# Kernel tuning notes

Hardware: AMD Instinct MI355X
Metric: run time of the kernel (lower is better)

## Reference

```python
import jax, jax.numpy as jnp
import numpy as np

# Static problem constants (see shape_source)
T_, H_, W_ = 8, 37, 37          # frames, feature-map height/width (518/14)
NH, MP = 8, 8                   # num_heads, max_points


def _point_mask_np():
    # n_points(t, r) = max(1, int(MP * (1 - |t-r|/(T-1)))) as in the TxT loop.
    d = np.abs(np.arange(T_)[:, None] - np.arange(T_)[None, :])
    n_p = np.maximum(1, (MP * (1.0 - d / (T_ - 1))).astype(np.int64))
    return np.arange(MP)[None, None, :] < n_p[:, :, None]   # [T, T, P] bool


def setup_inputs() -> dict:
    key = jax.random.key(0)
    ks = jax.random.split(key, 4)
    B, T, N, C = 2, T_, H_ * W_, 384
    f_bt = jax.random.normal(ks[0], (B, T, N, C), jnp.float32)
    Wq = 0.05 * jax.random.normal(ks[1], (C, C), jnp.float32)
    Woff = 0.1 * jax.random.normal(ks[2], (C, NH * MP * 2), jnp.float32)  # offsets span a few pixels
    Wout = 0.05 * jax.random.normal(ks[3], (C, C), jnp.float32)
    return {
        'f_bt': f_bt,
        'Wq': Wq, 'bq': jnp.zeros((C,), jnp.float32),
        'Woff': Woff, 'boff': jnp.zeros((NH * MP * 2,), jnp.float32),
        'Wout': Wout, 'bout': jnp.zeros((C,), jnp.float32),
    }


def _forward(f_bt, Wq, bq, Woff, boff, Wout, bout):
    B, T, N, C = f_bt.shape
    h, P = NH, MP
    hd = C // h
    scale = hd ** -0.5
    H, W = H_, W_

    # Per-frame projections (query and offsets depend only on t, computed once).
    q = (f_bt @ Wq + bq).reshape(B, T, N, h, hd)                 # [B,T,N,h,hd]
    off = (f_bt @ Woff + boff).reshape(B, T, N, h, P, 2)         # [B,T,N,h,P,2]

    ys, xs = jnp.meshgrid(jnp.arange(H), jnp.arange(W), indexing='ij')
    coords = jnp.stack([ys, xs], -1).reshape(N, 2).astype(f_bt.dtype)
    # Sampling locations in pixel space (align_corners=True normalize+denormalize is identity).
    loc = coords[None, None, :, None, None, :] + off             # [B,T,N,h,P,2]

    # Reference frames as per-head channel images, flattened spatially.
    ref = f_bt.transpose(0, 1, 3, 2).reshape(B, T, h, hd, N)     # [B,T,h,hd,H*W]
    mask = jnp.asarray(_point_mask_np())                         # [T,T,P]

    def attend(q_t, loc_t, mask_t):
        # q_t: [B,N,h,hd], loc_t: [B,N,h,P,2], mask_t: [T,P]
        y = loc_t[..., 0]
        x = loc_t[..., 1]
        y0f = jnp.floor(y)
        x0f = jnp.floor(x)
        wy = y - y0f
        wx = x - x0f

        def gather(yf, xf, w):
            yi = yf.astype(jnp.int32)
            xi = xf.astype(jnp.int32)
            valid = ((yi >= 0) & (yi < H) & (xi >= 0) & (xi < W)).astype(q_t.dtype)
            idx = jnp.clip(yi, 0, H - 1) * W + jnp.clip(xi, 0, W - 1)     # [B,N,h,P]
            idx = idx.transpose(0, 2, 1, 3).reshape(B, 1, h, 1, N * P)
            idx = jnp.broadcast_to(idx, (B, T, h, 1, N * P))
            vals = jnp.take_along_axis(ref, idx, axis=4)                   # [B,T,h,hd,N*P]
            vals = vals.reshape(B, T, h, hd, N, P)
            wv = (w * valid).transpose(0, 2, 1, 3)[:, None, :, None, :, :]  # [B,1,h,1,N,P]
            return vals * wv

        # Bilinear sample (zeros padding) of every reference frame at the
        # offset-predicted points of frame t.
        s = (gather(y0f, x0f, (1 - wy) * (1 - wx))
             + gather(y0f, x0f + 1, (1 - wy) * wx)
             + gather(y0f + 1, x0f, wy * (1 - wx))
             + gather(y0f + 1, x0f + 1, wy * wx))                # [B,T,h,hd,N,P]

        logits = jnp.einsum('bnhd,brhdnp->brnhp', q_t, s) * scale
        logits = logits + jnp.where(mask_t[None, :, None, None, :], 0.0, -1e30)
        attn = jax.nn.softmax(logits, axis=-1)
        out = jnp.einsum('brnhp,brhdnp->brnhd', attn, s).mean(axis=1)  # avg over T refs
        return out.reshape(B, N, C) @ Wout + bout

    body = jax.checkpoint(attend)

    def step(carry, xs):
        q_t, loc_t, mask_t = xs
        return carry, body(q_t, loc_t, mask_t)

    _, fused = jax.lax.scan(
        step, None,
        (q.transpose(1, 0, 2, 3, 4), loc.transpose(1, 0, 2, 3, 4, 5), mask))
    return fused.transpose(1, 0, 2, 3)   # [B,T,N,C]


def reference(f_bt, Wq, bq, Woff, boff, Wout, bout):
    return _forward(f_bt, Wq, bq, Woff, boff, Wout, bout)
```

## Files before the change

### kernel.cpp

```cpp
#include <hip/hip_runtime.h>
#include <hip/hip_bf16.h>
#include <hip/hip_fp16.h>
#include <cstddef>

constexpr int B_  = 2;
constexpr int T_  = 8;
constexpr int HW_ = 37;
constexpr int N_  = HW_ * HW_;
constexpr int C_  = 384;
constexpr int NH_ = 8;
constexpr int MP_ = 8;
constexpr int HD_ = C_ / NH_;
constexpr int M_  = B_ * T_ * N_;

typedef short bf16x8 __attribute__((ext_vector_type(8)));
typedef float f32x4 __attribute__((ext_vector_type(4)));
typedef float f32x2 __attribute__((ext_vector_type(2)));
typedef _Float16 h16x2 __attribute__((ext_vector_type(2)));
typedef unsigned u32x3 __attribute__((ext_vector_type(3)));
typedef u32x3 uau32x3 __attribute__((aligned(4)));

static __device__ __forceinline__ unsigned short bf16_bits(float v) {
  __hip_bfloat16 b = __float2bfloat16(v);
  return *reinterpret_cast<unsigned short*>(&b);
}

static __device__ __forceinline__ h16x2 bch2(unsigned u) {
  return __builtin_bit_cast(h16x2, u);
}

__global__ __launch_bounds__(256)
void cast_transpose_kernel(const float* __restrict__ f,
                           __hip_bfloat16* __restrict__ A16,
                           _Float16* __restrict__ ft) {
  const int bn = blockIdx.x;
  const int n = bn % N_;
  const int b = bn / N_;
  const size_t dst_base = (size_t)bn * (T_ * C_);
#pragma unroll
  for (int i = 0; i < 12; ++i) {
    int idx = i * 256 + threadIdx.x;
    int t = idx / C_;
    int c = idx - t * C_;
    size_t src = ((size_t)(b * T_ + t) * N_ + n) * C_ + c;
    float v = f[src];
    ft[dst_base + idx] = (_Float16)v;
    A16[src] = __float2bfloat16(v);
  }
}

__global__ __launch_bounds__(256)
void prep_w_kernel(const float* __restrict__ Wq, const float* __restrict__ Woff,
                   const float* __restrict__ Wout,
                   __hip_bfloat16* __restrict__ Wt, __hip_bfloat16* __restrict__ Wot) {
  int nrow = blockIdx.x;
  if (nrow < 512) {
    const float* src; int col, ld;
    if (nrow < 384) { src = Wq; col = nrow; ld = 384; }
    else            { src = Woff; col = nrow - 384; ld = 128; }
    for (int k = threadIdx.x; k < 384; k += 256)
      Wt[(size_t)nrow * 384 + k] = __float2bfloat16(src[(size_t)k * ld + col]);
  } else {
    int col = nrow - 512;
    for (int k = threadIdx.x; k < 384; k += 256)
      Wot[(size_t)col * 384 + k] = __float2bfloat16(Wout[(size_t)k * 384 + col]);
  }
}

__global__ __launch_bounds__(256)
void mfma_gemm_kernel(const __hip_bfloat16* __restrict__ A,
                      const __hip_bfloat16* __restrict__ Wt,
                      const float* __restrict__ b0, const float* __restrict__ b1,
                      float* __restrict__ out0, _Float16* __restrict__ out0h,
                      float* __restrict__ out1,
                      int split, float out0_scale) {
  __shared__ __hip_bfloat16 As[128][40];
  __shared__ __hip_bfloat16 Bs[128][40];
  const int m0 = blockIdx.x * 128;
  const int n0 = blockIdx.y * 128;
  const int tid = threadIdx.x;
  const int wv = tid >> 6, lane = tid & 63;
  const int wr = wv >> 1, wc = wv & 1;
  const int lr = lane & 15, kg = lane >> 4;

  f32x4 acc[4][4] = {};

  for (int k0 = 0; k0 < 384; k0 += 32) {
#pragma unroll
    for (int u = 0; u < 2; ++u) {
      int c = tid + u * 256;
      int row = c >> 2;
      int off = (c & 3) * 8;
      int gm = m0 + row;
      uint4 va = make_uint4(0u, 0u, 0u, 0u);
      if (gm < M_) va = *(const uint4*)(A + (size_t)gm * 384 + k0 + off);
      *(uint4*)&As[row][off] = va;
      uint4 vb = *(const uint4*)(Wt + (size_t)(n0 + row) * 384 + k0 + off);
      *(uint4*)&Bs[row][off] = vb;
    }
    __syncthreads();

    bf16x8 af[4], bfr[4];
#pragma unroll
    for (int i = 0; i < 4; ++i)
      af[i] = *(const bf16x8*)&As[wr * 64 + i * 16 + lr][kg * 8];
#pragma unroll
    for (int i = 0; i < 4; ++i)
      bfr[i] = *(const bf16x8*)&Bs[wc * 64 + i * 16 + lr][kg * 8];

#pragma unroll
    for (int mi = 0; mi < 4; ++mi)
#pragma unroll
      for (int ni = 0; ni < 4; ++ni)
        acc[mi][ni] = __builtin_amdgcn_mfma_f32_16x16x32_bf16(
            af[mi], bfr[ni], acc[mi][ni], 0, 0, 0);
    __syncthreads();
  }

  const int mrow = (lane >> 4) * 4;
#pragma unroll
  for (int mi = 0; mi < 4; ++mi) {
#pragma unroll
    for (int ni = 0; ni < 4; ++ni) {
#pragma unroll
      for (int j = 0; j < 4; ++j) {
        int gm = m0 + wr * 64 + mi * 16 + mrow + j;
        int gn = n0 + wc * 64 + ni * 16 + lr;
        if (gm >= M_) continue;
        float v = acc[mi][ni][j];
        if (!split) {
          out0[(size_t)gm * 384 + gn] = (v + b0[gn]) * out0_scale;
        } else {
          if (gn < 384) out0h[(size_t)gm * 384 + gn] =
              (_Float16)((v + b0[gn]) * out0_scale);
          else          out1[(size_t)gm * 128 + (gn - 384)] = v + b1[gn - 384];
        }
      }
    }
  }
}

__global__ __launch_bounds__(256)
void attend_kernel(const _Float16* __restrict__ ft,
                   const _Float16* __restrict__ Qh,
                   const float* __restrict__ OFF,
                   __hip_bfloat16* __restrict__ O1) {
  const int grid = B_ * N_ * 2;
  const int q8 = grid / 8, r8 = grid % 8;
  int c = blockIdx.x & 7, j = blockIdx.x >> 3;
  int id = (c < r8) ? c * (q8 + 1) + j : r8 * (q8 + 1) + (c - r8) * q8 + j;
  const int hq = id & 1;
  const int bn = id >> 1;

  const int n = bn % N_;
  const int b = bn / N_;
  const int w    = threadIdx.x >> 6;
  const int h    = hq * 4 + w;
  const int lane = threadIdx.x & 63;
  const int p = lane >> 3;
  const int k = lane & 7;
  const float cy = (float)(n / HW_);
  const float cx = (float)(n % HW_);
  const int bnb = b * N_;
  const int chb = h * HD_ + 6 * k;

  for (int t = 0; t < T_; ++t) {
    const size_t row = (size_t)(b * T_ + t) * N_ + n;

    uau32x3 qw = *(const uau32x3*)(Qh + row * C_ + h * HD_ + 6 * k);
    h16x2 q01 = bch2(qw.x), q23 = bch2(qw.y), q45 = bch2(qw.z);

    const float* op = OFF + row * (NH_ * MP_ * 2) + h * (MP_ * 2) + p * 2;
    float y = cy + op[0];
    float x = cx + op[1];
    float y0f = floorf(y), x0f = floorf(x);
    float wy = y - y0f, wx = x - x0f;
    int y0 = (int)y0f, x0 = (int)x0f;
    int y1 = y0 + 1, x1 = x0 + 1;
    float vy0 = (y0 >= 0 && y0 < HW_) ? 1.f : 0.f;
    float vy1 = (y1 >= 0 && y1 < HW_) ? 1.f : 0.f;
    float vx0 = (x0 >= 0 && x0 < HW_) ? 1.f : 0.f;
    float vx1 = (x1 >= 0 && x1 < HW_) ? 1.f : 0.f;
    int cy0 = min(max(y0, 0), HW_ - 1), cy1 = min(max(y1, 0), HW_ - 1);
    int cx0 = min(max(x0, 0), HW_ - 1), cx1 = min(max(x1, 0), HW_ - 1);
    float tw0 = (1.f - wy) * (1.f - wx) * vy0 * vx0;
    float tw1 = (1.f - wy) * wx * vy0 * vx1;
    float tw2 = wy * (1.f - wx) * vy1 * vx0;
    float tw3 = wy * wx * vy1 * vx1;
    _Float16 t0h = (_Float16)tw0, t1h = (_Float16)tw1;
    _Float16 t2h = (_Float16)tw2, t3h = (_Float16)tw3;
    h16x2 tw0h = {t0h, t0h}, tw1h = {t1h, t1h};
    h16x2 tw2h = {t2h, t2h}, tw3h = {t3h, t3h};

    const _Float16* tp0 = ft + ((bnb + cy0 * HW_ + cx0) * T_ + 3) * C_ + chb;
    const _Float16* tp1 = ft + ((bnb + cy0 * HW_ + cx1) * T_ + 3) * C_ + chb;
    const _Float16* tp2 = ft + ((bnb + cy1 * HW_ + cx0) * T_ + 3) * C_ + chb;
    const _Float16* tp3 = ft + ((bnb + cy1 * HW_ + cx1) * T_ + 3) * C_ + chb;

    float o0 = 0.f, o1 = 0.f, o2 = 0.f, o3 = 0.f, o4 = 0.f, o5 = 0.f;

#pragma unroll
    for (int r = 0; r < T_; ++r) {
      const int roff = (r - 3) * C_;
      uau32x3 ua = *(const uau32x3*)(tp0 + roff);
      uau32x3 ub = *(const uau32x3*)(tp1 + roff);
      uau32x3 uc = *(const uau32x3*)(tp2 + roff);
      uau32x3 ud = *(const uau32x3*)(tp3 + roff);

      h16x2 s01 = bch2(ua.x) * tw0h + bch2(ub.x) * tw1h + bch2(uc.x) * tw2h + bch2(ud.x) * tw3h;
      h16x2 s23 = bch2(ua.y) * tw0h + bch2(ub.y) * tw1h + bch2(uc.y) * tw2h + bch2(ud.y) * tw3h;
      h16x2 s45 = bch2(ua.z) * tw0h + bch2(ub.z) * tw1h + bch2(uc.z) * tw2h + bch2(ud.z) * tw3h;

      float lg = __builtin_amdgcn_fdot2(q01, s01,
                 __builtin_amdgcn_fdot2(q23, s23,
                 __builtin_amdgcn_fdot2(q45, s45, 0.f, false), false), false);
      lg += __shfl_xor(lg, 1);
      lg += __shfl_xor(lg, 2);
      lg += __shfl_xor(lg, 4);

      int dd = t - r; dd = dd < 0 ? -dd : dd;
      int npts = (56 - 8 * dd) / 7; npts = npts < 1 ? 1 : npts;

      float e = (p < npts) ? exp2f(lg) : 0.f;
      float ssum = e;
      ssum += __shfl_xor(ssum, 8);
      ssum += __shfl_xor(ssum, 16);
      ssum += __shfl_xor(ssum, 32);
      float attn = e * __builtin_amdgcn_rcpf(ssum);

      o0 = fmaf((float)s01.x, attn, o0);
      o1 = fmaf((float)s01.y, attn, o1);
      o2 = fmaf((float)s23.x, attn, o2);
      o3 = fmaf((float)s23.y, attn, o3);
      o4 = fmaf((float)s45.x, attn, o4);
      o5 = fmaf((float)s45.y, attn, o5);
    }

    o0 += __shfl_xor(o0, 8); o0 += __shfl_xor(o0, 16); o0 += __shfl_xor(o0, 32);
    o1 += __shfl_xor(o1, 8); o1 += __shfl_xor(o1, 16); o1 += __shfl_xor(o1, 32);
    o2 += __shfl_xor(o2, 8); o2 += __shfl_xor(o2, 16); o2 += __shfl_xor(o2, 32);
    o3 += __shfl_xor(o3, 8); o3 += __shfl_xor(o3, 16); o3 += __shfl_xor(o3, 32);
    o4 += __shfl_xor(o4, 8); o4 += __shfl_xor(o4, 16); o4 += __shfl_xor(o4, 32);
    o5 += __shfl_xor(o5, 8); o5 += __shfl_xor(o5, 16); o5 += __shfl_xor(o5, 32);

    if (p == 0) {
      __hip_bfloat16* outp = O1 + row * C_ + h * HD_ + 6 * k;
      unsigned* u = (unsigned*)outp;
      u[0] = (unsigned)bf16_bits(o0 * 0.125f) | ((unsigned)bf16_bits(o1 * 0.125f) << 16);
      u[1] = (unsigned)bf16_bits(o2 * 0.125f) | ((unsigned)bf16_bits(o3 * 0.125f) << 16);
      u[2] = (unsigned)bf16_bits(o4 * 0.125f) | ((unsigned)bf16_bits(o5 * 0.125f) << 16);
    }
  }
}

extern "C" void kernel_launch(void* const* d_in, const int* in_sizes, int n_in,
                              void* d_out, int out_size, void* d_ws, size_t ws_size,
                              hipStream_t stream) {
  const float* f    = (const float*)d_in[0];
  const float* Wq   = (const float*)d_in[1];
  const float* bq   = (const float*)d_in[2];
  const float* Woff = (const float*)d_in[3];
  const float* boff = (const float*)d_in[4];
  const float* Wout = (const float*)d_in[5];
  const float* bout = (const float*)d_in[6];
  float* outp = (float*)d_out;

  _Float16* Qh = (_Float16*)d_ws;
  float* OFFb = (float*)(Qh + (size_t)M_ * C_);
  _Float16* ft = (_Float16*)(OFFb + (size_t)M_ * 128);
  __hip_bfloat16* A16 = (__hip_bfloat16*)(ft + (size_t)B_ * N_ * T_ * C_);
  __hip_bfloat16* O1  = A16;
  __hip_bfloat16* Wt  = A16 + (size_t)M_ * C_;
  __hip_bfloat16* Wot = Wt + (size_t)512 * 384;

  dim3 blk(256);

  cast_transpose_kernel<<<dim3(B_ * N_), blk, 0, stream>>>(f, A16, ft);
  prep_w_kernel<<<dim3(896), blk, 0, stream>>>(Wq, Woff, Wout, Wt, Wot);

  mfma_gemm_kernel<<<dim3((M_ + 127) / 128, 4), blk, 0, stream>>>(
      A16, Wt, bq, boff, nullptr, Qh, OFFb, 1, 0.20822825268806912f);

  attend_kernel<<<dim3(B_ * N_ * 2), blk, 0, stream>>>(ft, Qh, OFFb, O1);

  mfma_gemm_kernel<<<dim3((M_ + 127) / 128, 3), blk, 0, stream>>>(
      O1, Wot, bout, nullptr, outp, nullptr, nullptr, 0, 1.0f);
}
```

Measured before the change: 323.0 us.

## Remap attend lanes to 4 channel groups x 8 points x 2 ref halves, accumulate in fp16

Reassigns each wavefront's lanes so that each lane covers 12 channels (4 lanes per head) and one of two reference-frame halves. The r loop drops from 8 to 4 iterations per lane, and the logit reduction needs fewer shuffles. The output accumulators become packed fp16 and are reduced with packed shuffles across points and ref halves, which halves the shuffle count. The cost is lower precision in the attention-weighted sum, since fp16 now accumulates across 64 terms, and more registers per lane for the wider loads.

```diff
diff --git a/kernel.cpp b/kernel.cpp
--- a/kernel.cpp
+++ b/kernel.cpp
@@ -27,6 +27,12 @@
 
 static __device__ __forceinline__ h16x2 bch2(unsigned u) {
   return __builtin_bit_cast(h16x2, u);
+}
+
+static __device__ __forceinline__ h16x2 pk_shfl_add(h16x2 v, int mask) {
+  unsigned u = __builtin_bit_cast(unsigned, v);
+  unsigned w = __shfl_xor(u, mask);
+  return v + __builtin_bit_cast(h16x2, w);
 }
 
 __global__ __launch_bounds__(256)
@@ -157,18 +163,22 @@
   const int w    = threadIdx.x >> 6;
   const int h    = hq * 4 + w;
   const int lane = threadIdx.x & 63;
-  const int p = lane >> 3;
-  const int k = lane & 7;
+  const int k4 = lane & 3;
+  const int p  = (lane >> 2) & 7;
+  const int rh = lane >> 5;
   const float cy = (float)(n / HW_);
   const float cx = (float)(n % HW_);
   const int bnb = b * N_;
-  const int chb = h * HD_ + 6 * k;
+  const int chb = h * HD_ + 12 * k4;
 
   for (int t = 0; t < T_; ++t) {
     const size_t row = (size_t)(b * T_ + t) * N_ + n;
 
-    uau32x3 qw = *(const uau32x3*)(Qh + row * C_ + h * HD_ + 6 * k);
-    h16x2 q01 = bch2(qw.x), q23 = bch2(qw.y), q45 = bch2(qw.z);
+    const _Float16* qp = Qh + row * C_ + chb;
+    uau32x3 qa = *(const uau32x3*)qp;
+    uau32x3 qb = *(const uau32x3*)(qp + 6);
+    h16x2 q0 = bch2(qa.x), q1 = bch2(qa.y), q2 = bch2(qa.z);
+    h16x2 q3 = bch2(qb.x), q4 = bch2(qb.y), q5 = bch2(qb.z);
 
     const float* op = OFF + row * (NH_ * MP_ * 2) + h * (MP_ * 2) + p * 2;
     float y = cy + op[0];
@@ -192,63 +202,79 @@
     h16x2 tw0h = {t0h, t0h}, tw1h = {t1h, t1h};
     h16x2 tw2h = {t2h, t2h}, tw3h = {t3h, t3h};
 
-    const _Float16* tp0 = ft + ((bnb + cy0 * HW_ + cx0) * T_ + 3) * C_ + chb;
-    const _Float16* tp1 = ft + ((bnb + cy0 * HW_ + cx1) * T_ + 3) * C_ + chb;
-    const _Float16* tp2 = ft + ((bnb + cy1 * HW_ + cx0) * T_ + 3) * C_ + chb;
-    const _Float16* tp3 = ft + ((bnb + cy1 * HW_ + cx1) * T_ + 3) * C_ + chb;
-
-    float o0 = 0.f, o1 = 0.f, o2 = 0.f, o3 = 0.f, o4 = 0.f, o5 = 0.f;
-
-#pragma unroll
-    for (int r = 0; r < T_; ++r) {
-      const int roff = (r - 3) * C_;
-      uau32x3 ua = *(const uau32x3*)(tp0 + roff);
-      uau32x3 ub = *(const uau32x3*)(tp1 + roff);
-      uau32x3 uc = *(const uau32x3*)(tp2 + roff);
-      uau32x3 ud = *(const uau32x3*)(tp3 + roff);
-
-      h16x2 s01 = bch2(ua.x) * tw0h + bch2(ub.x) * tw1h + bch2(uc.x) * tw2h + bch2(ud.x) * tw3h;
-      h16x2 s23 = bch2(ua.y) * tw0h + bch2(ub.y) * tw1h + bch2(uc.y) * tw2h + bch2(ud.y) * tw3h;
-      h16x2 s45 = bch2(ua.z) * tw0h + bch2(ub.z) * tw1h + bch2(uc.z) * tw2h + bch2(ud.z) * tw3h;
-
-      float lg = __builtin_amdgcn_fdot2(q01, s01,
-                 __builtin_amdgcn_fdot2(q23, s23,
-                 __builtin_amdgcn_fdot2(q45, s45, 0.f, false), false), false);
+    const _Float16* tp0 = ft + ((size_t)(bnb + cy0 * HW_ + cx0) * T_ + rh + 3) * C_ + chb;
+    const _Float16* tp1 = ft + ((size_t)(bnb + cy0 * HW_ + cx1) * T_ + rh + 3) * C_ + chb;
+    const _Float16* tp2 = ft + ((size_t)(bnb + cy1 * HW_ + cx0) * T_ + rh + 3) * C_ + chb;
+    const _Float16* tp3 = ft + ((size_t)(bnb + cy1 * HW_ + cx1) * T_ + rh + 3) * C_ + chb;
+
+    h16x2 o0 = {(_Float16)0.f, (_Float16)0.f}, o1 = o0, o2 = o0,
+          o3 = o0, o4 = o0, o5 = o0;
+
+#pragma unroll
+    for (int i = 0; i < 4; ++i) {
+      const int roff = (2 * i - 3) * C_;
+      uau32x3 a0 = *(const uau32x3*)(tp0 + roff);
+      uau32x3 a1 = *(const uau32x3*)(tp0 + roff + 6);
+      uau32x3 b0 = *(const uau32x3*)(tp1 + roff);
+      uau32x3 b1 = *(const uau32x3*)(tp1 + roff + 6);
+      uau32x3 c0 = *(const uau32x3*)(tp2 + roff);
+      uau32x3 c1 = *(const uau32x3*)(tp2 + roff + 6);
+      uau32x3 d0 = *(const uau32x3*)(tp3 + roff);
+      uau32x3 d1 = *(const uau32x3*)(tp3 + roff + 6);
+
+      h16x2 s0 = bch2(a0.x) * tw0h + bch2(b0.x) * tw1h + bch2(c0.x) * tw2h + bch2(d0.x) * tw3h;
+      h16x2 s1 = bch2(a0.y) * tw0h + bch2(b0.y) * tw1h + bch2(c0.y) * tw2h + bch2(d0.y) * tw3h;
+      h16x2 s2 = bch2(a0.z) * tw0h + bch2(b0.z) * tw1h + bch2(c0.z) * tw2h + bch2(d0.z) * tw3h;
+      h16x2 s3 = bch2(a1.x) * tw0h + bch2(b1.x) * tw1h + bch2(c1.x) * tw2h + bch2(d1.x) * tw3h;
+      h16x2 s4 = bch2(a1.y) * tw0h + bch2(b1.y) * tw1h + bch2(c1.y) * tw2h + bch2(d1.y) * tw3h;
+      h16x2 s5 = bch2(a1.z) * tw0h + bch2(b1.z) * tw1h + bch2(c1.z) * tw2h + bch2(d1.z) * tw3h;
+
+      float lg = __builtin_amdgcn_fdot2(q0, s0,
+                 __builtin_amdgcn_fdot2(q1, s1,
+                 __builtin_amdgcn_fdot2(q2, s2,
+                 __builtin_amdgcn_fdot2(q3, s3,
+                 __builtin_amdgcn_fdot2(q4, s4,
+                 __builtin_amdgcn_fdot2(q5, s5, 0.f, false),
+                 false), false), false), false), false);
+
       lg += __shfl_xor(lg, 1);
       lg += __shfl_xor(lg, 2);
-      lg += __shfl_xor(lg, 4);
-
+
+      int r = 2 * i + rh;
       int dd = t - r; dd = dd < 0 ? -dd : dd;
       int npts = (56 - 8 * dd) / 7; npts = npts < 1 ? 1 : npts;
 
       float e = (p < npts) ? exp2f(lg) : 0.f;
-      float ssum = e;
-      ssum += __shfl_xor(ssum, 8);
-      ssum += __shfl_xor(ssum, 16);
-      ssum += __shfl_xor(ssum, 32);
-      float attn = e * __builtin_amdgcn_rcpf(ssum);
-
-      o0 = fmaf((float)s01.x, attn, o0);
-      o1 = fmaf((float)s01.y, attn, o1);
-      o2 = fmaf((float)s23.x, attn, o2);
-      o3 = fmaf((float)s23.y, attn, o3);
-      o4 = fmaf((float)s45.x, attn, o4);
-      o5 = fmaf((float)s45.y, attn, o5);
-    }
-
-    o0 += __shfl_xor(o0, 8); o0 += __shfl_xor(o0, 16); o0 += __shfl_xor(o0, 32);
-    o1 += __shfl_xor(o1, 8); o1 += __shfl_xor(o1, 16); o1 += __shfl_xor(o1, 32);
-    o2 += __shfl_xor(o2, 8); o2 += __shfl_xor(o2, 16); o2 += __shfl_xor(o2, 32);
-    o3 += __shfl_xor(o3, 8); o3 += __shfl_xor(o3, 16); o3 += __shfl_xor(o3, 32);
-    o4 += __shfl_xor(o4, 8); o4 += __shfl_xor(o4, 16); o4 += __shfl_xor(o4, 32);
-    o5 += __shfl_xor(o5, 8); o5 += __shfl_xor(o5, 16); o5 += __shfl_xor(o5, 32);
-
-    if (p == 0) {
-      __hip_bfloat16* outp = O1 + row * C_ + h * HD_ + 6 * k;
-      unsigned* u = (unsigned*)outp;
-      u[0] = (unsigned)bf16_bits(o0 * 0.125f) | ((unsigned)bf16_bits(o1 * 0.125f) << 16);
-      u[1] = (unsigned)bf16_bits(o2 * 0.125f) | ((unsigned)bf16_bits(o3 * 0.125f) << 16);
-      u[2] = (unsigned)bf16_bits(o4 * 0.125f) | ((unsigned)bf16_bits(o5 * 0.125f) << 16);
+      float ss = e + __shfl_xor(e, 4);
+      ss += __shfl_xor(ss, 8);
+      ss += __shfl_xor(ss, 16);
+      float attn = e * __builtin_amdgcn_rcpf(ss);
+
+      _Float16 ah = (_Float16)attn;
+      h16x2 av = {ah, ah};
+      o0 += av * s0; o1 += av * s1; o2 += av * s2;
+      o3 += av * s3; o4 += av * s4; o5 += av * s5;
+    }
+
+#pragma unroll
+    for (int m = 4; m <= 32; m <<= 1) {
+      o0 = pk_shfl_add(o0, m); o1 = pk_shfl_add(o1, m);
+      o2 = pk_shfl_add(o2, m); o3 = pk_shfl_add(o3, m);
+      o4 = pk_shfl_add(o4, m); o5 = pk_shfl_add(o5, m);
+    }
+
+    if ((lane >> 2) == 0) {
+      __hip_bfloat16* outp = O1 + row * C_ + chb;
+      unsigned u[6];
+      u[0] = (unsigned)bf16_bits((float)o0.x * 0.125f) | ((unsigned)bf16_bits((float)o0.y * 0.125f) << 16);
+      u[1] = (unsigned)bf16_bits((float)o1.x * 0.125f) | ((unsigned)bf16_bits((float)o1.y * 0.125f) << 16);
+      u[2] = (unsigned)bf16_bits((float)o2.x * 0.125f) | ((unsigned)bf16_bits((float)o2.y * 0.125f) << 16);
+      u[3] = (unsigned)bf16_bits((float)o3.x * 0.125f) | ((unsigned)bf16_bits((float)o3.y * 0.125f) << 16);
+      u[4] = (unsigned)bf16_bits((float)o4.x * 0.125f) | ((unsigned)bf16_bits((float)o4.y * 0.125f) << 16);
+      u[5] = (unsigned)bf16_bits((float)o5.x * 0.125f) | ((unsigned)bf16_bits((float)o5.y * 0.125f) << 16);
+      unsigned* up = (unsigned*)outp;
+      up[0] = u[0]; up[1] = u[1]; up[2] = u[2];
+      up[3] = u[3]; up[4] = u[4]; up[5] = u[5];
     }
   }
 }
```

Result: slower. 547.6 us (+69.5%).

## Reorder feature layout per head and swap lane mapping to reference frames

Applied to the files above, without the earlier changes.

The cast kernel now writes the fp16 reference features as [b, head, pixel, frame, 48], so all 8 frames of one head at one pixel form one contiguous 768-byte block. In the attend kernel each 8-lane group now handles one reference frame and loops over the 8 sampling points, so a wavefront's gather of one bilinear corner is a single contiguous load. Softmax normalisation moves out of the loop: exponentials and their sum are accumulated per lane and the output is scaled once, which drops the per-iteration cross-lane sum reductions. The cost is recomputing the bilinear weights and addresses for each point in every lane group, plus a scattered write pattern in the cast kernel.

```diff
diff --git a/kernel.cpp b/kernel.cpp
--- a/kernel.cpp
+++ b/kernel.cpp
@@ -32,19 +32,20 @@
 __global__ __launch_bounds__(256)
 void cast_transpose_kernel(const float* __restrict__ f,
                            __hip_bfloat16* __restrict__ A16,
-                           _Float16* __restrict__ ft) {
+                           _Float16* __restrict__ fth) {
   const int bn = blockIdx.x;
   const int n = bn % N_;
   const int b = bn / N_;
-  const size_t dst_base = (size_t)bn * (T_ * C_);
 #pragma unroll
   for (int i = 0; i < 12; ++i) {
     int idx = i * 256 + threadIdx.x;
     int t = idx / C_;
     int c = idx - t * C_;
+    int h = c / HD_;
+    int c48 = c - h * HD_;
     size_t src = ((size_t)(b * T_ + t) * N_ + n) * C_ + c;
     float v = f[src];
-    ft[dst_base + idx] = (_Float16)v;
+    fth[(((size_t)(b * NH_ + h) * N_ + n) * T_ + t) * HD_ + c48] = (_Float16)v;
     A16[src] = __float2bfloat16(v);
   }
 }
@@ -141,7 +142,7 @@
 }
 
 __global__ __launch_bounds__(256)
-void attend_kernel(const _Float16* __restrict__ ft,
+void attend_kernel(const _Float16* __restrict__ fth,
                    const _Float16* __restrict__ Qh,
                    const float* __restrict__ OFF,
                    __hip_bfloat16* __restrict__ O1) {
@@ -157,12 +158,13 @@
   const int w    = threadIdx.x >> 6;
   const int h    = hq * 4 + w;
   const int lane = threadIdx.x & 63;
-  const int p = lane >> 3;
+  const int r = lane >> 3;
   const int k = lane & 7;
   const float cy = (float)(n / HW_);
   const float cx = (float)(n % HW_);
-  const int bnb = b * N_;
-  const int chb = h * HD_ + 6 * k;
+
+  const _Float16* fh = fth + (size_t)(b * NH_ + h) * N_ * (T_ * HD_);
+  const int laneoff = lane * 6;
 
   for (int t = 0; t < T_; ++t) {
     const size_t row = (size_t)(b * T_ + t) * N_ + n;
@@ -170,42 +172,45 @@
     uau32x3 qw = *(const uau32x3*)(Qh + row * C_ + h * HD_ + 6 * k);
     h16x2 q01 = bch2(qw.x), q23 = bch2(qw.y), q45 = bch2(qw.z);
 
-    const float* op = OFF + row * (NH_ * MP_ * 2) + h * (MP_ * 2) + p * 2;
-    float y = cy + op[0];
-    float x = cx + op[1];
-    float y0f = floorf(y), x0f = floorf(x);
-    float wy = y - y0f, wx = x - x0f;
-    int y0 = (int)y0f, x0 = (int)x0f;
-    int y1 = y0 + 1, x1 = x0 + 1;
-    float vy0 = (y0 >= 0 && y0 < HW_) ? 1.f : 0.f;
-    float vy1 = (y1 >= 0 && y1 < HW_) ? 1.f : 0.f;
-    float vx0 = (x0 >= 0 && x0 < HW_) ? 1.f : 0.f;
-    float vx1 = (x1 >= 0 && x1 < HW_) ? 1.f : 0.f;
-    int cy0 = min(max(y0, 0), HW_ - 1), cy1 = min(max(y1, 0), HW_ - 1);
-    int cx0 = min(max(x0, 0), HW_ - 1), cx1 = min(max(x1, 0), HW_ - 1);
-    float tw0 = (1.f - wy) * (1.f - wx) * vy0 * vx0;
-    float tw1 = (1.f - wy) * wx * vy0 * vx1;
-    float tw2 = wy * (1.f - wx) * vy1 * vx0;
-    float tw3 = wy * wx * vy1 * vx1;
-    _Float16 t0h = (_Float16)tw0, t1h = (_Float16)tw1;
-    _Float16 t2h = (_Float16)tw2, t3h = (_Float16)tw3;
-    h16x2 tw0h = {t0h, t0h}, tw1h = {t1h, t1h};
-    h16x2 tw2h = {t2h, t2h}, tw3h = {t3h, t3h};
-
-    const _Float16* tp0 = ft + ((bnb + cy0 * HW_ + cx0) * T_ + 3) * C_ + chb;
-    const _Float16* tp1 = ft + ((bnb + cy0 * HW_ + cx1) * T_ + 3) * C_ + chb;
-    const _Float16* tp2 = ft + ((bnb + cy1 * HW_ + cx0) * T_ + 3) * C_ + chb;
-    const _Float16* tp3 = ft + ((bnb + cy1 * HW_ + cx1) * T_ + 3) * C_ + chb;
+    int dd = t - r; dd = dd < 0 ? -dd : dd;
+    const int npts = max(1, (56 - 8 * dd) / 7);
+
+    const float* opb = OFF + row * (NH_ * MP_ * 2) + h * (MP_ * 2);
 
     float o0 = 0.f, o1 = 0.f, o2 = 0.f, o3 = 0.f, o4 = 0.f, o5 = 0.f;
-
-#pragma unroll
-    for (int r = 0; r < T_; ++r) {
-      const int roff = (r - 3) * C_;
-      uau32x3 ua = *(const uau32x3*)(tp0 + roff);
-      uau32x3 ub = *(const uau32x3*)(tp1 + roff);
-      uau32x3 uc = *(const uau32x3*)(tp2 + roff);
-      uau32x3 ud = *(const uau32x3*)(tp3 + roff);
+    float esum = 0.f;
+
+#pragma unroll
+    for (int p = 0; p < MP_; ++p) {
+      float y = cy + opb[2 * p];
+      float x = cx + opb[2 * p + 1];
+      float y0f = floorf(y), x0f = floorf(x);
+      float wy = y - y0f, wx = x - x0f;
+      int y0 = (int)y0f, x0 = (int)x0f;
+      int y1 = y0 + 1, x1 = x0 + 1;
+      float vy0 = (y0 >= 0 && y0 < HW_) ? 1.f : 0.f;
+      float vy1 = (y1 >= 0 && y1 < HW_) ? 1.f : 0.f;
+      float vx0 = (x0 >= 0 && x0 < HW_) ? 1.f : 0.f;
+      float vx1 = (x1 >= 0 && x1 < HW_) ? 1.f : 0.f;
+      int cy0 = min(max(y0, 0), HW_ - 1), cy1 = min(max(y1, 0), HW_ - 1);
+      int cx0 = min(max(x0, 0), HW_ - 1), cx1 = min(max(x1, 0), HW_ - 1);
+      float tw0 = (1.f - wy) * (1.f - wx) * vy0 * vx0;
+      float tw1 = (1.f - wy) * wx * vy0 * vx1;
+      float tw2 = wy * (1.f - wx) * vy1 * vx0;
+      float tw3 = wy * wx * vy1 * vx1;
+      _Float16 t0h = (_Float16)tw0, t1h = (_Float16)tw1;
+      _Float16 t2h = (_Float16)tw2, t3h = (_Float16)tw3;
+      h16x2 tw0h = {t0h, t0h}, tw1h = {t1h, t1h};
+      h16x2 tw2h = {t2h, t2h}, tw3h = {t3h, t3h};
+
+      const _Float16* g0 = fh + (size_t)(cy0 * HW_ + cx0) * (T_ * HD_) + laneoff;
+      const _Float16* g1 = fh + (size_t)(cy0 * HW_ + cx1) * (T_ * HD_) + laneoff;
+      const _Float16* g2 = fh + (size_t)(cy1 * HW_ + cx0) * (T_ * HD_) + laneoff;
+      const _Float16* g3 = fh + (size_t)(cy1 * HW_ + cx1) * (T_ * HD_) + laneoff;
+      uau32x3 ua = *(const uau32x3*)g0;
+      uau32x3 ub = *(const uau32x3*)g1;
+      uau32x3 uc = *(const uau32x3*)g2;
+      uau32x3 ud = *(const uau32x3*)g3;
 
       h16x2 s01 = bch2(ua.x) * tw0h + bch2(ub.x) * tw1h + bch2(uc.x) * tw2h + bch2(ud.x) * tw3h;
       h16x2 s23 = bch2(ua.y) * tw0h + bch2(ub.y) * tw1h + bch2(uc.y) * tw2h + bch2(ud.y) * tw3h;
@@ -218,23 +223,19 @@
       lg += __shfl_xor(lg, 2);
       lg += __shfl_xor(lg, 4);
 
-      int dd = t - r; dd = dd < 0 ? -dd : dd;
-      int npts = (56 - 8 * dd) / 7; npts = npts < 1 ? 1 : npts;
-
       float e = (p < npts) ? exp2f(lg) : 0.f;
-      float ssum = e;
-      ssum += __shfl_xor(ssum, 8);
-      ssum += __shfl_xor(ssum, 16);
-      ssum += __shfl_xor(ssum, 32);
-      float attn = e * __builtin_amdgcn_rcpf(ssum);
-
-      o0 = fmaf((float)s01.x, attn, o0);
-      o1 = fmaf((float)s01.y, attn, o1);
-      o2 = fmaf((float)s23.x, attn, o2);
-      o3 = fmaf((float)s23.y, attn, o3);
-      o4 = fmaf((float)s45.x, attn, o4);
-      o5 = fmaf((float)s45.y, attn, o5);
-    }
+      esum += e;
+
+      o0 = fmaf((float)s01.x, e, o0);
+      o1 = fmaf((float)s01.y, e, o1);
+      o2 = fmaf((float)s23.x, e, o2);
+      o3 = fmaf((float)s23.y, e, o3);
+      o4 = fmaf((float)s45.x, e, o4);
+      o5 = fmaf((float)s45.y, e, o5);
+    }
+
+    float inv = __builtin_amdgcn_rcpf(esum);
+    o0 *= inv; o1 *= inv; o2 *= inv; o3 *= inv; o4 *= inv; o5 *= inv;
 
     o0 += __shfl_xor(o0, 8); o0 += __shfl_xor(o0, 16); o0 += __shfl_xor(o0, 32);
     o1 += __shfl_xor(o1, 8); o1 += __shfl_xor(o1, 16); o1 += __shfl_xor(o1, 32);
@@ -243,7 +244,7 @@
     o4 += __shfl_xor(o4, 8); o4 += __shfl_xor(o4, 16); o4 += __shfl_xor(o4, 32);
     o5 += __shfl_xor(o5, 8); o5 += __shfl_xor(o5, 16); o5 += __shfl_xor(o5, 32);
 
-    if (p == 0) {
+    if (r == 0) {
       __hip_bfloat16* outp = O1 + row * C_ + h * HD_ + 6 * k;
       unsigned* u = (unsigned*)outp;
       u[0] = (unsigned)bf16_bits(o0 * 0.125f) | ((unsigned)bf16_bits(o1 * 0.125f) << 16);
@@ -267,21 +268,21 @@
 
   _Float16* Qh = (_Float16*)d_ws;
   float* OFFb = (float*)(Qh + (size_t)M_ * C_);
-  _Float16* ft = (_Float16*)(OFFb + (size_t)M_ * 128);
-  __hip_bfloat16* A16 = (__hip_bfloat16*)(ft + (size_t)B_ * N_ * T_ * C_);
+  _Float16* fth = (_Float16*)(OFFb + (size_t)M_ * 128);
+  __hip_bfloat16* A16 = (__hip_bfloat16*)(fth + (size_t)B_ * N_ * T_ * C_);
   __hip_bfloat16* O1  = A16;
   __hip_bfloat16* Wt  = A16 + (size_t)M_ * C_;
   __hip_bfloat16* Wot = Wt + (size_t)512 * 384;
 
   dim3 blk(256);
 
-  cast_transpose_kernel<<<dim3(B_ * N_), blk, 0, stream>>>(f, A16, ft);
+  cast_transpose_kernel<<<dim3(B_ * N_), blk, 0, stream>>>(f, A16, fth);
   prep_w_kernel<<<dim3(896), blk, 0, stream>>>(Wq, Woff, Wout, Wt, Wot);
 
   mfma_gemm_kernel<<<dim3((M_ + 127) / 128, 4), blk, 0, stream>>>(
       A16, Wt, bq, boff, nullptr, Qh, OFFb, 1, 0.20822825268806912f);
 
-  attend_kernel<<<dim3(B_ * N_ * 2), blk, 0, stream>>>(ft, Qh, OFFb, O1);
+  attend_kernel<<<dim3(B_ * N_ * 2), blk, 0, stream>>>(fth, Qh, OFFb, O1);
 
   mfma_gemm_kernel<<<dim3((M_ + 127) / 128, 3), blk, 0, stream>>>(
       O1, Wot, bout, nullptr, outp, nullptr, nullptr, 0, 1.0f);
```

Measured after the change: 312.4 us. 3.3% less time.
